# Optimization experiments

Hardware: AMD Instinct MI355X
Metric: run time of the kernel (lower is better)

The kernel has to match this reference:

```python
import jax, jax.numpy as jnp
import numpy as np

# RadixAttention EXTEND forward: queries over newly-extended tokens attend to
# (a) the full cached prefix KV (non-causal) and (b) the extend-token KV (causal),
# equivalent to attention over concat([prefix, extend]) with a shifted causal mask.

SCALING = 0.08838834764831845  # 1/sqrt(128)


def setup_inputs() -> dict:
    key = jax.random.key(0)
    k1, k2, k3, k4, k5 = jax.random.split(key, 5)
    B, E, P, H, Hk, D = 4, 512, 1536, 32, 8, 128
    return {
        "q": jax.random.normal(k1, (B, E, H, D), dtype=jnp.float32),
        "k": jax.random.normal(k2, (B, E, Hk, D), dtype=jnp.float32),
        "v": jax.random.normal(k3, (B, E, Hk, D), dtype=jnp.float32),
        "k_cache": jax.random.normal(k4, (B, P, Hk, D), dtype=jnp.float32),
        "v_cache": jax.random.normal(k5, (B, P, Hk, D), dtype=jnp.float32),
    }


def reference(q, k, v, k_cache, v_cache):
    B, E, H, D = q.shape
    Hk = k.shape[2]
    P = k_cache.shape[1]
    g = H // Hk  # GQA group size
    S = P + E

    k_all = jnp.concatenate([k_cache, k], axis=1)  # [B, S, Hk, D]
    v_all = jnp.concatenate([v_cache, v], axis=1)  # [B, S, Hk, D]

    qg = q.reshape(B, E, Hk, g, D)
    # scores: [B, Hk, g, E, S]
    scores = jnp.einsum("bekgd,bskd->bkges", qg, k_all) * SCALING

    # key j visible to extend-query e iff j <= P + e (prefix fully visible, extend causal)
    visible = jnp.arange(S)[None, :] <= (P + jnp.arange(E))[:, None]  # [E, S]
    scores = jnp.where(visible[None, None, None, :, :], scores, jnp.float32(-1e30))

    p = jax.nn.softmax(scores, axis=-1)
    o = jnp.einsum("bkges,bskd->bekgd", p, v_all).reshape(B, E, H, D)
    # module returns flat [num_tokens, H*D]
    return o.reshape(B * E, H * D)
```

## Files before the change

kernel.cpp:

```cpp
#include <hip/hip_runtime.h>
#include <hip/hip_bf16.h>
#include <stdint.h>
#include <stddef.h>


#define B_ 4
#define E_ 512
#define P_ 1536
#define H_ 32
#define HK_ 8
#define D_ 128
#define G_ 4
#define S_ 2048

#define BLOCK_E 32
#define NT 64
#define PPITCH 72
#define TPITCH 72
#define KVSTRIDE (HK_ * D_)
#define NTHREADS 256
#define M_FIX 12.0f

typedef __attribute__((ext_vector_type(8))) short short8v;
typedef __attribute__((ext_vector_type(4))) float floatx4;

__device__ __forceinline__ short2 f2bf2(float a, float b) {
  __hip_bfloat162 h = __float22bfloat162_rn(float2{a, b});
  return *(short2*)&h;
}
__device__ __forceinline__ short f2bf(float f) {
  union { float f; uint32_t u; } x; x.f = f;
  uint32_t r = x.u + 0x7FFFu + ((x.u >> 16) & 1u);
  return (short)(r >> 16);
}
__device__ __forceinline__ short8v cvt8(const float4 a, const float4 b) {
  short2 p0 = f2bf2(a.x, a.y), p1 = f2bf2(a.z, a.w);
  short2 p2 = f2bf2(b.x, b.y), p3 = f2bf2(b.z, b.w);
  short8v f;
  f[0] = p0.x; f[1] = p0.y; f[2] = p1.x; f[3] = p1.y;
  f[4] = p2.x; f[5] = p2.y; f[6] = p3.x; f[7] = p3.y;
  return f;
}

__global__ __launch_bounds__(256)
void prep_kv(const float* __restrict__ kc, const float* __restrict__ ke,
             const float* __restrict__ vc, const float* __restrict__ ve,
             short* __restrict__ kb, short* __restrict__ vt) {
  __shared__ short TT[D_ * TPITCH];
  const int bid = blockIdx.x;
  const int tid = threadIdx.x;
  if (bid < 4096) {
    const int cid = bid * 256 + tid;
    const int d8c = cid & 15;
    const int j   = (cid >> 4) & (S_ - 1);
    const int kh  = (cid >> 15) & 7;
    const int b   = cid >> 18;
    const float* src = (j < P_)
        ? (kc + (((size_t)b * P_ + j) * HK_ + kh) * D_ + d8c * 8)
        : (ke + (((size_t)b * E_ + (j - P_)) * HK_ + kh) * D_ + d8c * 8);
    const float4 x0 = *(const float4*)src;
    const float4 x1 = *(const float4*)(src + 4);
    *(short8v*)&kb[(((size_t)b * HK_ + kh) * S_ + j) * D_ + d8c * 8] = cvt8(x0, x1);
  } else {
    const int b2 = bid - 4096;
    const int j0 = (b2 & 31) * 64;
    const int kh = (b2 >> 5) & 7;
    const int b  = b2 >> 8;
#pragma unroll
    for (int it = 0; it < 8; ++it) {
      const int linear = it * 256 + tid;
      const int key = linear >> 5;
      const int dof = (linear & 31) * 4;
      const int j = j0 + key;
      const float* src = (j < P_)
          ? (vc + (((size_t)b * P_ + j) * HK_ + kh) * D_ + dof)
          : (ve + (((size_t)b * E_ + (j - P_)) * HK_ + kh) * D_ + dof);
      const float4 x = *(const float4*)src;
      short2 a = f2bf2(x.x, x.y), c = f2bf2(x.z, x.w);
      TT[(dof + 0) * TPITCH + key] = a.x;
      TT[(dof + 1) * TPITCH + key] = a.y;
      TT[(dof + 2) * TPITCH + key] = c.x;
      TT[(dof + 3) * TPITCH + key] = c.y;
    }
    __syncthreads();
#pragma unroll
    for (int it = 0; it < 4; ++it) {
      const int linear = it * 256 + tid;
      const int d  = linear >> 3;
      const int k8 = (linear & 7) * 8;
      *(short8v*)&vt[(((size_t)b * HK_ + kh) * D_ + d) * S_ + j0 + k8] =
          *(const short8v*)&TT[d * TPITCH + k8];
    }
  }
}

__global__ __launch_bounds__(NTHREADS, 2)
void radix_attn(const float* __restrict__ q,
                const short* __restrict__ kb,
                const short* __restrict__ vt,
                float* __restrict__ out) {
  __shared__ short KT[2][NT * D_];
  __shared__ short VTs[2][D_ * NT];
  __shared__ short PW[4][16 * PPITCH];

  const int flat = blockIdx.x;
  const int kh   = flat & 7;
  const int b    = (flat >> 3) & 3;
  const int e0   = (flat >> 5) * BLOCK_E;
  const int tid  = threadIdx.x;
  const int wave = tid >> 6;
  const int lane = tid & 63;
  const int quad = lane >> 4;
  const int l16  = lane & 15;
  const int h    = kh * G_ + wave;

  short8v qf[2][4];
#pragma unroll
  for (int rb = 0; rb < 2; ++rb) {
    const int e = e0 + rb * 16 + l16;
    const float* qp = q + (((size_t)b * E_ + e) * H_ + h) * D_ + quad * 8;
#pragma unroll
    for (int kcc = 0; kcc < 4; ++kcc)
      qf[rb][kcc] = cvt8(*(const float4*)(qp + kcc * 32), *(const float4*)(qp + kcc * 32 + 4));
  }

  short8v ones8;
#pragma unroll
  for (int i = 0; i < 8; ++i) ones8[i] = (l16 == 0) ? (short)0x3F80 : (short)0;

  floatx4 oacc[2][8];
#pragma unroll
  for (int rb = 0; rb < 2; ++rb)
#pragma unroll
    for (int dt = 0; dt < 8; ++dt) oacc[rb][dt] = (floatx4){0.f, 0.f, 0.f, 0.f};
  floatx4 acc_l[2] = {(floatx4){0.f, 0.f, 0.f, 0.f}, (floatx4){0.f, 0.f, 0.f, 0.f}};

  const short* kbb = kb + ((size_t)b * HK_ + kh) * S_ * D_;
  const short* vtb = vt + ((size_t)b * HK_ + kh) * (size_t)D_ * S_;

  const int slimit = P_ + e0 + BLOCK_E;
  const int ntiles = (slimit + NT - 1) / NT;
  const float sc = 0.08838834764831845f * 1.44269504088896340f;

  short8v kpre[4], vpre[4];
  auto preload = [&](int t) {
    const int kt0 = t * NT;
#pragma unroll
    for (int it = 0; it < 4; ++it) {
      const int c = it * 256 + tid;
      const int key = c >> 4, cl = c & 15;
      kpre[it] = *(const short8v*)&kbb[(size_t)(kt0 + key) * D_ + cl * 8];
    }
#pragma unroll
    for (int it = 0; it < 4; ++it) {
      const int c = it * 256 + tid;
      const int d = c >> 3, ck = c & 7;
      vpre[it] = *(const short8v*)&vtb[(size_t)d * S_ + kt0 + ck * 8];
    }
  };
  auto stage = [&](int buf) {
#pragma unroll
    for (int it = 0; it < 4; ++it) {
      const int c = it * 256 + tid;
      const int key = c >> 4, cl = c & 15;
      const int cs = ((cl & 7) ^ (key & 7)) | (cl & 8);
      *(short8v*)&KT[buf][key * D_ + cs * 8] = kpre[it];
    }
#pragma unroll
    for (int it = 0; it < 4; ++it) {
      const int c = it * 256 + tid;
      const int d = c >> 3, ck = c & 7;
      *(short8v*)&VTs[buf][d * NT + (ck ^ (d & 7)) * 8] = vpre[it];
    }
  };

  preload(0);
  stage(0);
  if (ntiles > 1) preload(1);
  __syncthreads();

  for (int t = 0; t < ntiles; ++t) {
    const int kt0 = t * NT;
    const int cur = t & 1;

    if (t + 1 < ntiles) stage(cur ^ 1);
    if (t + 2 < ntiles) preload(t + 2);

    floatx4 sfr[2][4];
#pragma unroll
    for (int nc = 0; nc < 4; ++nc) {
      short8v kf[4];
#pragma unroll
      for (int kcc = 0; kcc < 4; ++kcc) {
        const int cl = kcc * 4 + quad;
        const int cs = ((cl & 7) ^ (l16 & 7)) | (cl & 8);
        kf[kcc] = *(const short8v*)&KT[cur][(nc * 16 + l16) * D_ + cs * 8];
      }
#pragma unroll
      for (int rb = 0; rb < 2; ++rb) {
        floatx4 acc = (floatx4){0.f, 0.f, 0.f, 0.f};
#pragma unroll
        for (int kcc = 0; kcc < 4; ++kcc)
          acc = __builtin_amdgcn_mfma_f32_16x16x32_bf16(kf[kcc], qf[rb][kcc], acc, 0, 0, 0);
        sfr[rb][nc] = acc;
      }
    }

    short8v pf[2][2];
#pragma unroll
    for (int rb = 0; rb < 2; ++rb) {
      const bool need_mask = (kt0 + NT - 1 > P_ + e0 + rb * 16);
      const int qlim = P_ + e0 + rb * 16 + l16;
#pragma unroll
      for (int nc = 0; nc < 4; ++nc) {
        float p[4];
#pragma unroll
        for (int reg = 0; reg < 4; ++reg) {
          float pe = __builtin_amdgcn_exp2f(__builtin_fmaf(sfr[rb][nc][reg], sc, -M_FIX));
          if (need_mask) {
            const int jkey = kt0 + nc * 16 + quad * 4 + reg;
            if (jkey > qlim) pe = 0.f;
          }
          p[reg] = pe;
        }
        const short2 a = f2bf2(p[0], p[1]), c = f2bf2(p[2], p[3]);
        short4 y; y.x = a.x; y.y = a.y; y.z = c.x; y.w = c.y;
        *(short4*)&PW[wave][l16 * PPITCH + nc * 16 + quad * 4] = y;
      }
#pragma unroll
      for (int kc = 0; kc < 2; ++kc)
        pf[rb][kc] = *(const short8v*)&PW[wave][l16 * PPITCH + kc * 32 + quad * 8];
    }

#pragma unroll
    for (int kc = 0; kc < 2; ++kc) {
#pragma unroll
      for (int dt = 0; dt < 8; ++dt) {
        const int cs = (kc * 4 + quad) ^ (l16 & 7);
        const short8v vf = *(const short8v*)&VTs[cur][(dt * 16 + l16) * NT + cs * 8];
#pragma unroll
        for (int rb = 0; rb < 2; ++rb)
          oacc[rb][dt] = __builtin_amdgcn_mfma_f32_16x16x32_bf16(pf[rb][kc], vf, oacc[rb][dt], 0, 0, 0);
      }
#pragma unroll
      for (int rb = 0; rb < 2; ++rb)
        acc_l[rb] = __builtin_amdgcn_mfma_f32_16x16x32_bf16(pf[rb][kc], ones8, acc_l[rb], 0, 0, 0);
    }
    __syncthreads();
  }

#pragma unroll
  for (int rb = 0; rb < 2; ++rb) {
    float inv[4];
#pragma unroll
    for (int reg = 0; reg < 4; ++reg) {
      const float l = __shfl(acc_l[rb][reg], lane & 48, 64);
      inv[reg] = 1.0f / l;
    }
#pragma unroll
    for (int reg = 0; reg < 4; ++reg) {
      const int erow = e0 + rb * 16 + quad * 4 + reg;
      float* op = out + (size_t)(b * E_ + erow) * (H_ * D_) + h * D_ + l16;
#pragma unroll
      for (int dt = 0; dt < 8; ++dt)
        op[dt * 16] = oacc[rb][dt][reg] * inv[reg];
    }
  }
}

__global__ __launch_bounds__(1024, 4)
void radix_attn_fp32(const float* __restrict__ q,
                     const float* __restrict__ ke,
                     const float* __restrict__ ve,
                     const float* __restrict__ kc,
                     const float* __restrict__ vc,
                     float* __restrict__ out) {
  __shared__ short KT[NT * 136];
  __shared__ short VTs[D_ * TPITCH];
  __shared__ short PW[16][16 * 80];
  const int flat = blockIdx.x;
  const int kh = flat & 7, b = (flat >> 3) & 3, e0 = (flat >> 5) * 64;
  const int tid = threadIdx.x, wave = tid >> 6, lane = tid & 63;
  const int quad = lane >> 4, l16 = lane & 15;
  const int gi = wave & 3, rbw = wave >> 2, h = kh * G_ + gi;
  short8v qf[4];
  {
    const int e = e0 + rbw * 16 + l16;
    const float* qp = q + (((size_t)b * E_ + e) * H_ + h) * D_ + quad * 8;
#pragma unroll
    for (int kcc = 0; kcc < 4; ++kcc)
      qf[kcc] = cvt8(*(const float4*)(qp + kcc * 32), *(const float4*)(qp + kcc * 32 + 4));
  }
  short8v ones8;
#pragma unroll
  for (int i = 0; i < 8; ++i) ones8[i] = (l16 == 0) ? (short)0x3F80 : (short)0;
  floatx4 oacc[8];
#pragma unroll
  for (int d = 0; d < 8; ++d) oacc[d] = (floatx4){0.f, 0.f, 0.f, 0.f};
  floatx4 acc_l = (floatx4){0.f, 0.f, 0.f, 0.f};
  float mrow[4];
#pragma unroll
  for (int r = 0; r < 4; ++r) mrow[r] = -1e30f;
  const float* kcb = kc + (size_t)b * P_ * KVSTRIDE + (size_t)kh * D_;
  const float* keb = ke + (size_t)b * E_ * KVSTRIDE + (size_t)kh * D_;
  const float* vcb = vc + (size_t)b * P_ * KVSTRIDE + (size_t)kh * D_;
  const float* veb = ve + (size_t)b * E_ * KVSTRIDE + (size_t)kh * D_;
  const int ntiles = (P_ + e0 + 64) / NT;
  const float sc = 0.08838834764831845f * 1.44269504088896340f;
  for (int t = 0; t < ntiles; ++t) {
    const int kt0 = t * NT;
    __syncthreads();
#pragma unroll
    for (int it = 0; it < 2; ++it) {
      const int linear = it * 1024 + tid;
      const int key = linear >> 5, dof = (linear & 31) * 4;
      const int j = kt0 + key;
      const float* src = (j < P_) ? (kcb + (size_t)j * KVSTRIDE) : (keb + (size_t)(j - P_) * KVSTRIDE);
      const float4 x = *(const float4*)(src + dof);
      short2 a = f2bf2(x.x, x.y), c = f2bf2(x.z, x.w);
      short4 y; y.x = a.x; y.y = a.y; y.z = c.x; y.w = c.y;
      *(short4*)&KT[key * 136 + dof] = y;
    }
#pragma unroll
    for (int it = 0; it < 2; ++it) {
      const int linear = it * 1024 + tid;
      const int key = linear & 63, dg = (linear >> 6) * 4;
      const int j = kt0 + key;
      const float* src = (j < P_) ? (vcb + (size_t)j * KVSTRIDE) : (veb + (size_t)(j - P_) * KVSTRIDE);
      const float4 x = *(const float4*)(src + dg);
      short2 a = f2bf2(x.x, x.y), c = f2bf2(x.z, x.w);
      VTs[(dg + 0) * TPITCH + key] = a.x;
      VTs[(dg + 1) * TPITCH + key] = a.y;
      VTs[(dg + 2) * TPITCH + key] = c.x;
      VTs[(dg + 3) * TPITCH + key] = c.y;
    }
    __syncthreads();
    floatx4 sfr[4];
#pragma unroll
    for (int nc = 0; nc < 4; ++nc) {
      floatx4 acc = (floatx4){0.f, 0.f, 0.f, 0.f};
#pragma unroll
      for (int kcc = 0; kcc < 4; ++kcc) {
        const short8v bf = *(const short8v*)&KT[(nc * 16 + l16) * 136 + kcc * 32 + quad * 8];
        acc = __builtin_amdgcn_mfma_f32_16x16x32_bf16(qf[kcc], bf, acc, 0, 0, 0);
      }
      sfr[nc] = acc;
    }
    const bool need_mask = (kt0 + NT - 1 > P_ + e0 + rbw * 16);
#pragma unroll
    for (int nc = 0; nc < 4; ++nc)
#pragma unroll
      for (int reg = 0; reg < 4; ++reg) {
        float s = sfr[nc][reg] * sc;
        if (need_mask) {
          const int jkey = kt0 + nc * 16 + l16;
          const int erow = e0 + rbw * 16 + quad * 4 + reg;
          if (jkey > P_ + erow) s = -1e30f;
        }
        sfr[nc][reg] = s;
      }
    float mt[4];
#pragma unroll
    for (int reg = 0; reg < 4; ++reg)
      mt[reg] = fmaxf(fmaxf(sfr[0][reg], sfr[1][reg]), fmaxf(sfr[2][reg], sfr[3][reg]));
#pragma unroll
    for (int off = 1; off < 16; off <<= 1)
#pragma unroll
      for (int reg = 0; reg < 4; ++reg)
        mt[reg] = fmaxf(mt[reg], __shfl_xor(mt[reg], off, 64));
#pragma unroll
    for (int reg = 0; reg < 4; ++reg) {
      const float mnew = fmaxf(mrow[reg], mt[reg]);
      const float alpha = __builtin_amdgcn_exp2f(mrow[reg] - mnew);
      mrow[reg] = mnew;
      acc_l[reg] *= alpha;
#pragma unroll
      for (int d = 0; d < 8; ++d) oacc[d][reg] *= alpha;
    }
#pragma unroll
    for (int nc = 0; nc < 4; ++nc)
#pragma unroll
      for (int reg = 0; reg < 4; ++reg) {
        const float p = __builtin_amdgcn_exp2f(sfr[nc][reg] - mrow[reg]);
        PW[wave][(quad * 4 + reg) * 80 + nc * 16 + l16] = f2bf(p);
      }
    const short8v pf0 = *(const short8v*)&PW[wave][l16 * 80 + quad * 8];
    const short8v pf1 = *(const short8v*)&PW[wave][l16 * 80 + 32 + quad * 8];
#pragma unroll
    for (int d = 0; d < 8; ++d) {
      const short8v vf0 = *(const short8v*)&VTs[(d * 16 + l16) * TPITCH + quad * 8];
      const short8v vf1 = *(const short8v*)&VTs[(d * 16 + l16) * TPITCH + 32 + quad * 8];
      oacc[d] = __builtin_amdgcn_mfma_f32_16x16x32_bf16(pf0, vf0, oacc[d], 0, 0, 0);
      oacc[d] = __builtin_amdgcn_mfma_f32_16x16x32_bf16(pf1, vf1, oacc[d], 0, 0, 0);
    }
    acc_l = __builtin_amdgcn_mfma_f32_16x16x32_bf16(pf0, ones8, acc_l, 0, 0, 0);
    acc_l = __builtin_amdgcn_mfma_f32_16x16x32_bf16(pf1, ones8, acc_l, 0, 0, 0);
  }
  float inv[4];
#pragma unroll
  for (int reg = 0; reg < 4; ++reg)
    inv[reg] = 1.0f / __shfl(acc_l[reg], lane & 48, 64);
#pragma unroll
  for (int reg = 0; reg < 4; ++reg) {
    const int erow = e0 + rbw * 16 + quad * 4 + reg;
    float* op = out + (size_t)(b * E_ + erow) * (H_ * D_) + h * D_ + l16;
#pragma unroll
    for (int d = 0; d < 8; ++d)
      op[d * 16] = oacc[d][reg] * inv[reg];
  }
}

extern "C" void kernel_launch(void* const* d_in, const int* in_sizes, int n_in,
                              void* d_out, int out_size, void* d_ws, size_t ws_size,
                              hipStream_t stream) {
  const float* q  = (const float*)d_in[0];
  const float* ke = (const float*)d_in[1];
  const float* ve = (const float*)d_in[2];
  const float* kc = (const float*)d_in[3];
  const float* vc = (const float*)d_in[4];
  float* out = (float*)d_out;

  const size_t kv_shorts = (size_t)B_ * HK_ * S_ * D_;
  const size_t need = 2 * kv_shorts * sizeof(short);

  if (ws_size >= need) {
    short* kb = (short*)d_ws;
    short* vt = kb + kv_shorts;
    prep_kv<<<dim3(4096 + 1024), dim3(256), 0, stream>>>(kc, ke, vc, ve, kb, vt);
    const int nblk = (E_ / BLOCK_E) * HK_ * B_;
    radix_attn<<<dim3(nblk), dim3(NTHREADS), 0, stream>>>(q, kb, vt, out);
  } else {
    radix_attn_fp32<<<dim3(8 * 8 * 4), dim3(1024), 0, stream>>>(q, ke, ve, kc, vc, out);
  }
}
```

Baseline: 219.0 us.

## Pre-tile swizzled KV in prep kernel and stream tiles via direct global-to-LDS loads

The prep kernel now writes K and transposed V in per-tile contiguous, pre-swizzled 16KB blocks matching the LDS layout. The attention kernel then loads each tile straight into LDS with global_load_lds, replacing the register preload and LDS store staging. Half the V fragments are also read early to overlap with the softmax, and the barrier moves to the top of the loop. This removes register pressure and VGPR-to-LDS store traffic, but leaves only one tile of prefetch distance and relies on the implicit wait at the barrier for the async loads to complete.

```diff
diff --git a/kernel.cpp b/kernel.cpp
--- a/kernel.cpp
+++ b/kernel.cpp
@@ -20,6 +20,7 @@
 #define KVSTRIDE (HK_ * D_)
 #define NTHREADS 256
 #define M_FIX 12.0f
+#define TILE_SHORTS 8192
 
 typedef __attribute__((ext_vector_type(8))) short short8v;
 typedef __attribute__((ext_vector_type(4))) float floatx4;
@@ -51,16 +52,19 @@
   const int tid = threadIdx.x;
   if (bid < 4096) {
     const int cid = bid * 256 + tid;
-    const int d8c = cid & 15;
+    const int cl  = cid & 15;
     const int j   = (cid >> 4) & (S_ - 1);
     const int kh  = (cid >> 15) & 7;
     const int b   = cid >> 18;
     const float* src = (j < P_)
-        ? (kc + (((size_t)b * P_ + j) * HK_ + kh) * D_ + d8c * 8)
-        : (ke + (((size_t)b * E_ + (j - P_)) * HK_ + kh) * D_ + d8c * 8);
+        ? (kc + (((size_t)b * P_ + j) * HK_ + kh) * D_ + cl * 8)
+        : (ke + (((size_t)b * E_ + (j - P_)) * HK_ + kh) * D_ + cl * 8);
     const float4 x0 = *(const float4*)src;
     const float4 x1 = *(const float4*)(src + 4);
-    *(short8v*)&kb[(((size_t)b * HK_ + kh) * S_ + j) * D_ + d8c * 8] = cvt8(x0, x1);
+    const int t = j >> 6, key = j & 63;
+    const int cs = ((cl & 7) ^ (key & 7)) | (cl & 8);
+    *(short8v*)&kb[(((size_t)(b * 8 + kh) * 32 + t)) * TILE_SHORTS + key * 128 + cs * 8] =
+        cvt8(x0, x1);
   } else {
     const int b2 = bid - 4096;
     const int j0 = (b2 & 31) * 64;
@@ -87,9 +91,10 @@
     for (int it = 0; it < 4; ++it) {
       const int linear = it * 256 + tid;
       const int d  = linear >> 3;
-      const int k8 = (linear & 7) * 8;
-      *(short8v*)&vt[(((size_t)b * HK_ + kh) * D_ + d) * S_ + j0 + k8] =
-          *(const short8v*)&TT[d * TPITCH + k8];
+      const int ck = linear & 7;
+      const int cks = ck ^ (d & 7);
+      *(short8v*)&vt[(((size_t)(b * 8 + kh) * 32 + (j0 >> 6))) * TILE_SHORTS + d * 64 + cks * 8] =
+          *(const short8v*)&TT[d * TPITCH + ck * 8];
     }
   }
 }
@@ -135,56 +140,37 @@
     for (int dt = 0; dt < 8; ++dt) oacc[rb][dt] = (floatx4){0.f, 0.f, 0.f, 0.f};
   floatx4 acc_l[2] = {(floatx4){0.f, 0.f, 0.f, 0.f}, (floatx4){0.f, 0.f, 0.f, 0.f}};
 
-  const short* kbb = kb + ((size_t)b * HK_ + kh) * S_ * D_;
-  const short* vtb = vt + ((size_t)b * HK_ + kh) * (size_t)D_ * S_;
+  const short* kbt = kb + (size_t)(b * 8 + kh) * 32 * TILE_SHORTS;
+  const short* vtt = vt + (size_t)(b * 8 + kh) * 32 * TILE_SHORTS;
 
   const int slimit = P_ + e0 + BLOCK_E;
   const int ntiles = (slimit + NT - 1) / NT;
   const float sc = 0.08838834764831845f * 1.44269504088896340f;
 
-  short8v kpre[4], vpre[4];
-  auto preload = [&](int t) {
-    const int kt0 = t * NT;
-#pragma unroll
-    for (int it = 0; it < 4; ++it) {
-      const int c = it * 256 + tid;
-      const int key = c >> 4, cl = c & 15;
-      kpre[it] = *(const short8v*)&kbb[(size_t)(kt0 + key) * D_ + cl * 8];
-    }
-#pragma unroll
-    for (int it = 0; it < 4; ++it) {
-      const int c = it * 256 + tid;
-      const int d = c >> 3, ck = c & 7;
-      vpre[it] = *(const short8v*)&vtb[(size_t)d * S_ + kt0 + ck * 8];
+  auto dma = [&](int t, int buf) {
+    const char* kg = (const char*)kbt + (size_t)t * 16384 + wave * 4096 + lane * 16;
+    const char* vg = (const char*)vtt + (size_t)t * 16384 + wave * 4096 + lane * 16;
+    short* kl = &KT[buf][wave * 2048];
+    short* vl = &VTs[buf][wave * 2048];
+#pragma unroll
+    for (int g = 0; g < 4; ++g) {
+      __builtin_amdgcn_global_load_lds(
+          (const __attribute__((address_space(1))) void*)(kg + g * 1024),
+          (__attribute__((address_space(3))) void*)(kl + g * 512), 16, 0, 0);
+      __builtin_amdgcn_global_load_lds(
+          (const __attribute__((address_space(1))) void*)(vg + g * 1024),
+          (__attribute__((address_space(3))) void*)(vl + g * 512), 16, 0, 0);
     }
   };
-  auto stage = [&](int buf) {
-#pragma unroll
-    for (int it = 0; it < 4; ++it) {
-      const int c = it * 256 + tid;
-      const int key = c >> 4, cl = c & 15;
-      const int cs = ((cl & 7) ^ (key & 7)) | (cl & 8);
-      *(short8v*)&KT[buf][key * D_ + cs * 8] = kpre[it];
-    }
-#pragma unroll
-    for (int it = 0; it < 4; ++it) {
-      const int c = it * 256 + tid;
-      const int d = c >> 3, ck = c & 7;
-      *(short8v*)&VTs[buf][d * NT + (ck ^ (d & 7)) * 8] = vpre[it];
-    }
-  };
-
-  preload(0);
-  stage(0);
-  if (ntiles > 1) preload(1);
-  __syncthreads();
+
+  dma(0, 0);
 
   for (int t = 0; t < ntiles; ++t) {
     const int kt0 = t * NT;
     const int cur = t & 1;
 
-    if (t + 1 < ntiles) stage(cur ^ 1);
-    if (t + 2 < ntiles) preload(t + 2);
+    __syncthreads();
+    if (t + 1 < ntiles) dma(t + 1, cur ^ 1);
 
     floatx4 sfr[2][4];
 #pragma unroll
@@ -205,6 +191,15 @@
         sfr[rb][nc] = acc;
       }
     }
+
+    short8v vfr[2][4];
+#pragma unroll
+    for (int kc = 0; kc < 2; ++kc)
+#pragma unroll
+      for (int dt = 0; dt < 4; ++dt) {
+        const int cs = (kc * 4 + quad) ^ (l16 & 7);
+        vfr[kc][dt] = *(const short8v*)&VTs[cur][(dt * 16 + l16) * NT + cs * 8];
+      }
 
     short8v pf[2][2];
 #pragma unroll
@@ -236,8 +231,13 @@
     for (int kc = 0; kc < 2; ++kc) {
 #pragma unroll
       for (int dt = 0; dt < 8; ++dt) {
-        const int cs = (kc * 4 + quad) ^ (l16 & 7);
-        const short8v vf = *(const short8v*)&VTs[cur][(dt * 16 + l16) * NT + cs * 8];
+        short8v vf;
+        if (dt < 4) {
+          vf = vfr[kc][dt];
+        } else {
+          const int cs = (kc * 4 + quad) ^ (l16 & 7);
+          vf = *(const short8v*)&VTs[cur][(dt * 16 + l16) * NT + cs * 8];
+        }
 #pragma unroll
         for (int rb = 0; rb < 2; ++rb)
           oacc[rb][dt] = __builtin_amdgcn_mfma_f32_16x16x32_bf16(pf[rb][kc], vf, oacc[rb][dt], 0, 0, 0);
@@ -246,7 +246,6 @@
       for (int rb = 0; rb < 2; ++rb)
         acc_l[rb] = __builtin_amdgcn_mfma_f32_16x16x32_bf16(pf[rb][kc], ones8, acc_l[rb], 0, 0, 0);
     }
-    __syncthreads();
   }
 
 #pragma unroll
```

Measured after the change: 212.7 us. 2.8% less time.
